# Optimization experiments

Measured on AMD Instinct MI355X. Metric: run time of the kernel, lower is better.

Reference implementation:

```python
import jax, jax.numpy as jnp
import numpy as np

H_RES, W_RES = 32, 32
DIM = 512
NUM_HEADS = 16
HEAD_DIM = DIM // NUM_HEADS
SCALE = HEAD_DIM ** -0.5
B = 16
N = H_RES * W_RES
TABLE_SIZE = (2 * H_RES - 1) * (2 * W_RES - 1)


def _relative_position_index():
    coords_h = np.arange(H_RES)
    coords_w = np.arange(W_RES)
    coords = np.stack(np.meshgrid(coords_h, coords_w, indexing='ij'))  # [2, H, W]
    coords_flat = coords.reshape(2, -1)  # [2, N]
    rel = coords_flat[:, :, None] - coords_flat[:, None, :]  # [2, N, N]
    rel = rel.transpose(1, 2, 0).astype(np.int64)  # [N, N, 2]
    rel[:, :, 0] += H_RES - 1
    rel[:, :, 1] += W_RES - 1
    rel[:, :, 0] *= 2 * W_RES - 1
    return rel.sum(-1)  # [N, N]


def setup_inputs() -> dict:
    key = jax.random.key(0)
    ks = jax.random.split(key, 6)
    x = jax.random.normal(ks[0], (B, N, DIM), dtype=jnp.float32)
    w_qkv = jax.random.normal(ks[1], (DIM, 3 * DIM), dtype=jnp.float32) * (DIM ** -0.5)
    b_qkv = jnp.zeros((3 * DIM,), dtype=jnp.float32)
    w_proj = jax.random.normal(ks[2], (DIM, DIM), dtype=jnp.float32) * (DIM ** -0.5)
    b_proj = jnp.zeros((DIM,), dtype=jnp.float32)
    bias_table = jax.random.normal(ks[3], (TABLE_SIZE, NUM_HEADS), dtype=jnp.float32) * 0.02
    rel_index = jnp.asarray(_relative_position_index(), dtype=jnp.int32)
    return {"x": x, "w_qkv": w_qkv, "b_qkv": b_qkv, "w_proj": w_proj,
            "b_proj": b_proj, "bias_table": bias_table, "rel_index": rel_index}


def reference(x, w_qkv, b_qkv, w_proj, b_proj, bias_table, rel_index):
    Bq, Nq, C = x.shape
    qkv = x @ w_qkv + b_qkv  # [B, N, 3C]
    qkv = qkv.reshape(Bq, Nq, 3, NUM_HEADS, HEAD_DIM)
    q = qkv[:, :, 0].transpose(0, 2, 1, 3) * SCALE  # [B, nH, N, d]
    k = qkv[:, :, 1].transpose(0, 2, 1, 3)
    v = qkv[:, :, 2].transpose(0, 2, 1, 3)
    attn = jnp.einsum('bhnd,bhmd->bhnm', q, k)  # [B, nH, N, N]
    bias = bias_table[rel_index]  # [N, N, nH]
    attn = attn + bias.transpose(2, 0, 1)[None]  # broadcast over batch
    attn = jax.nn.softmax(attn, axis=-1)
    out = jnp.einsum('bhnm,bhmd->bhnd', attn, v)  # [B, nH, N, d]
    out = out.transpose(0, 2, 1, 3).reshape(Bq, Nq, C)
    return out @ w_proj + b_proj
```

## Files before the change

kernel.cpp:

```cpp
#include <hip/hip_runtime.h>
#include <hip/hip_bf16.h>
#include <cstdint>
#include <cstddef>

typedef _Float16 f16;
typedef __attribute__((ext_vector_type(8))) _Float16 f16x8;
typedef __attribute__((ext_vector_type(2))) _Float16 f16x2;
typedef __bf16 bf16;
typedef __attribute__((ext_vector_type(4))) float f32x4;
typedef __attribute__((ext_vector_type(16))) float f32x16;

#define LOG2E 1.4426950408889634f
#define QK_SCALE 0.17677669529663687f

__device__ __forceinline__ f32x4 mfma16f(f16x8 a, f16x8 b, f32x4 c) {
  return __builtin_amdgcn_mfma_f32_16x16x32_f16(a, b, c, 0, 0, 0);
}
__device__ __forceinline__ f32x16 mfma32f(f16x8 a, f16x8 b, f32x16 c) {
  return __builtin_amdgcn_mfma_f32_32x32x16_f16(a, b, c, 0, 0, 0);
}
__device__ __forceinline__ float exp2_hw(float x) {
  float r; asm("v_exp_f32 %0, %1" : "=v"(r) : "v"(x)); return r;
}
__device__ __forceinline__ uint32_t cvtpk_f16(float a, float b) {
  uint32_t r; asm("v_cvt_pkrtz_f16_f32 %0, %1, %2" : "=v"(r) : "v"(a), "v"(b)); return r;
}
__device__ __forceinline__ float lo16f(uint32_t u) { return __uint_as_float(u << 16); }
__device__ __forceinline__ float hi16f(uint32_t u) { return __uint_as_float(u & 0xFFFF0000u); }

__device__ __forceinline__ float dot2acc(uint32_t u, float acc) {
  union { uint32_t x; f16x2 h; } c; c.x = u;
  f16x2 one2 = {(_Float16)1.0f, (_Float16)1.0f};
  return __builtin_amdgcn_fdot2(c.h, one2, acc, false);
}

__device__ __forceinline__ void gl16(const f16* g, f16* l) {
  __builtin_amdgcn_global_load_lds(
      (const __attribute__((address_space(1))) void*)g,
      (__attribute__((address_space(3))) void*)l, 16, 0, 0);
}

__device__ __forceinline__ uint32_t packoff(int m, int k) {
  return (((uint32_t)(m >> 7) * 16u + (uint32_t)(k >> 5)) * 8u + (uint32_t)((m >> 4) & 7)) * 512u
       + (uint32_t)((k >> 3) & 3) * 128u + (uint32_t)(m & 15) * 8u + (uint32_t)(k & 7);
}

__global__ __launch_bounds__(256) void prep_kernel(
    const float* __restrict__ x, const float* __restrict__ wqkv, const float* __restrict__ wproj,
    f16* __restrict__ Xp, f16* __restrict__ Wq, f16* __restrict__ Wp)
{
  const int XT  = 16384 * 512 / 16;
  const int WQT = 1536 * 512 / 16;
  int t = blockIdx.x * 256 + threadIdx.x;
  if (t < XT) {
    uint32_t o = (uint32_t)t * 16u;
    uint32_t blk = o >> 9, rem = o & 511u;
    uint32_t k23 = rem >> 7, r16 = (rem >> 3) & 15u;
    uint32_t i7 = blk & 7u, k5 = (blk >> 3) & 15u, m7 = blk >> 7;
    uint32_t m = m7 * 128u + i7 * 16u + r16;
    uint32_t k = k5 * 32u + k23 * 8u;
    const float* s0 = x + (size_t)m * 512 + k;
    f32x4 a0 = *(const f32x4*)s0;
    f32x4 a1 = *(const f32x4*)(s0 + 4);
    f32x4 b0 = *(const f32x4*)(s0 + 512);
    f32x4 b1 = *(const f32x4*)(s0 + 516);
    f16 ov[16];
    #pragma unroll
    for (int j = 0; j < 4; ++j) {
      ov[j] = (f16)a0[j]; ov[4 + j] = (f16)a1[j];
      ov[8 + j] = (f16)b0[j]; ov[12 + j] = (f16)b1[j];
    }
    *(uint4*)(Xp + o) = *(uint4*)&ov[0];
    *(uint4*)(Xp + o + 8) = *(uint4*)&ov[8];
  } else if (t < XT + WQT) {
    uint32_t o = (uint32_t)(t - XT) * 16u;
    uint32_t blk = o >> 9, rem = o & 511u;
    uint32_t k23 = rem >> 7, r16 = (rem >> 3) & 15u;
    uint32_t i7 = blk & 7u, k5 = (blk >> 3) & 15u, m7 = blk >> 7;
    uint32_t n = m7 * 128u + i7 * 16u + r16;
    uint32_t k = k5 * 32u + k23 * 8u;
    f16 ov[16];
    #pragma unroll
    for (int j = 0; j < 8; ++j) {
      ov[j] = (f16)wqkv[(size_t)(k + j) * 1536 + n];
      ov[8 + j] = (f16)wqkv[(size_t)(k + j) * 1536 + n + 1];
    }
    *(uint4*)(Wq + o) = *(uint4*)&ov[0];
    *(uint4*)(Wq + o + 8) = *(uint4*)&ov[8];
  } else {
    uint32_t o = (uint32_t)(t - XT - WQT) * 16u;
    uint32_t blk = o >> 9, rem = o & 511u;
    uint32_t k23 = rem >> 7, r16 = (rem >> 3) & 15u;
    uint32_t i7 = blk & 7u, k5 = (blk >> 3) & 15u, m7 = blk >> 7;
    uint32_t n = m7 * 128u + i7 * 16u + r16;
    uint32_t k = k5 * 32u + k23 * 8u;
    f16 ov[16];
    #pragma unroll
    for (int j = 0; j < 8; ++j) {
      ov[j] = (f16)wproj[(size_t)(k + j) * 512 + n];
      ov[8 + j] = (f16)wproj[(size_t)(k + j) * 512 + n + 1];
    }
    *(uint4*)(Wp + o) = *(uint4*)&ov[0];
    *(uint4*)(Wp + o + 8) = *(uint4*)&ov[8];
  }
}

__global__ __launch_bounds__(256) void tblT_kernel(
    const float* __restrict__ btab, float* __restrict__ tblT)
{
  int e = blockIdx.x * 256 + threadIdx.x;
  if (e < 3969 * 16) {
    int h = e & 15, i = e >> 4;
    tblT[h * 4000 + i] = btab[e] * LOG2E;
  }
}

__global__ __launch_bounds__(256) void biasC_kernel(
    const float* __restrict__ tblT, bf16* __restrict__ biasC)
{
  int t = blockIdx.x * 256 + threadIdx.x;
  if (t >= 16 * 63 * 64) return;
  int lane = t & 63;
  int sh = t >> 6;
  int s = sh % 63, h = sh / 63;
  int lq = lane & 31, hi5 = lane >> 5;
  const float* row = tblT + h * 4000 + s * 63 + 31 + lq;
  bf16 o[16];
  #pragma unroll
  for (int r = 0; r < 16; ++r) {
    int kx = (r & 3) + 8 * (r >> 2) + 4 * hi5;
    o[r] = (bf16)row[-kx];
  }
  *(uint4*)(biasC + (size_t)t * 16) = *(uint4*)&o[0];
  *(uint4*)(biasC + (size_t)t * 16 + 8) = *(uint4*)&o[8];
}

template<int NB>
__global__ __launch_bounds__(256) void gemm_frag(
    const f16* __restrict__ Ap, const f16* __restrict__ Bp,
    const float* __restrict__ bvec,
    f16* __restrict__ Qp, f16* __restrict__ Kp, f16* __restrict__ Vt,
    float* __restrict__ out)
{
  __shared__ f16 sA[3][4096];
  __shared__ f16 sB[3][4096];
  const int bid = blockIdx.x;
  const int xcd = bid & 7, idx = bid >> 3;
  int mb, nb;
  if (NB == 12) { int q = idx / 12; mb = xcd * 16 + q; nb = idx - q * 12; }
  else          { mb = xcd * 16 + (idx >> 2); nb = idx & 3; }
  const int tid = threadIdx.x, lane = tid & 63, wave = tid >> 6;
  const int l15 = lane & 15, l4 = lane >> 4;
  const int wr = wave >> 1, wc = wave & 1;

  const f16* gA = Ap + (uint32_t)mb * 65536u + (uint32_t)wave * 1024u + (uint32_t)lane * 8u;
  const f16* gB = Bp + (uint32_t)nb * 65536u + (uint32_t)wave * 1024u + (uint32_t)lane * 8u;
  const int wl = wave * 1024;

  gl16(gA,        &sA[0][wl]);
  gl16(gA + 512,  &sA[0][wl + 512]);
  gl16(gB,        &sB[0][wl]);
  gl16(gB + 512,  &sB[0][wl + 512]);
  gl16(gA + 4096, &sA[1][wl]);
  gl16(gA + 4608, &sA[1][wl + 512]);
  gl16(gB + 4096, &sB[1][wl]);
  gl16(gB + 4608, &sB[1][wl + 512]);

  f32x4 acc[4][4];
  #pragma unroll
  for (int i = 0; i < 4; ++i)
    #pragma unroll
    for (int j = 0; j < 4; ++j) acc[i][j] = (f32x4){0.f, 0.f, 0.f, 0.f};

  const uint32_t aoff = (uint32_t)(wr * 4) * 512u + (uint32_t)lane * 8u;
  const uint32_t boff = (uint32_t)(wc * 4) * 512u + (uint32_t)lane * 8u;

  #pragma unroll
  for (int kt = 0; kt < 16; ++kt) {
    asm volatile("s_waitcnt vmcnt(4)" ::: "memory");
    asm volatile("s_barrier" ::: "memory");
    const int s0 = kt % 3;
    f16x8 af[4], bfr[4];
    #pragma unroll
    for (int f = 0; f < 4; ++f) {
      af[f]  = *(const f16x8*)&sA[s0][aoff + f * 512];
      bfr[f] = *(const f16x8*)&sB[s0][boff + f * 512];
    }
    const int s2 = (kt + 2) % 3;
    gl16(gA + (kt + 2) * 4096,       &sA[s2][wl]);
    gl16(gA + (kt + 2) * 4096 + 512, &sA[s2][wl + 512]);
    gl16(gB + (kt + 2) * 4096,       &sB[s2][wl]);
    gl16(gB + (kt + 2) * 4096 + 512, &sB[s2][wl + 512]);
    #pragma unroll
    for (int mf = 0; mf < 4; ++mf)
      #pragma unroll
      for (int nf = 0; nf < 4; ++nf)
        acc[mf][nf] = mfma16f(af[mf], bfr[nf], acc[mf][nf]);
  }
  asm volatile("s_waitcnt vmcnt(0)" ::: "memory");

  #pragma unroll
  for (int mf = 0; mf < 4; ++mf) {
    #pragma unroll
    for (int nf = 0; nf < 4; ++nf) {
      int colb = nb * 128 + wc * 64 + nf * 16 + l15;
      float bb = bvec[colb];
      #pragma unroll
      for (int i = 0; i < 4; ++i) {
        int m = mb * 128 + wr * 64 + mf * 16 + l4 * 4 + i;
        float v = acc[mf][nf][i] + bb;
        if (NB == 4) {
          out[(size_t)m * 512 + colb] = v;
        } else {
          int t = colb >> 9, cc = colb & 511;
          int b = m >> 10, n = m & 1023;
          int hh = cc >> 5, d = cc & 31;
          int bh2 = b * 16 + hh;
          if (t == 0) {
            v *= (QK_SCALE * LOG2E);
            uint32_t off = (((uint32_t)bh2 * 32u + (uint32_t)(n >> 5)) * 2u + (uint32_t)(d >> 4)) * 512u
                         + ((uint32_t)((d >> 3) & 1) * 32u + (uint32_t)(n & 31)) * 8u + (uint32_t)(d & 7);
            Qp[off] = (f16)v;
          } else if (t == 1) {
            Kp[((size_t)(bh2 * 2 + (d >> 4)) * 1024 + n) * 16 + (d & 15)] = (f16)v;
          } else {
            int nl = n & 15;
            int npl = (nl >= 4 && nl < 12) ? (nl ^ 12) : nl;
            int np = (n & ~15) | npl;
            Vt[((size_t)(bh2 * 128 + (np >> 3)) * 32 + d) * 8 + (np & 7)] = (f16)v;
          }
        }
      }
    }
  }
}

__global__ __launch_bounds__(256) void attn_kernel(
    const f16* __restrict__ Qp, const f16* __restrict__ Kp, const f16* __restrict__ Vt,
    const bf16* __restrict__ biasC, f16* __restrict__ Op)
{
  const int bid = blockIdx.x;
  const int xcd = bid & 7, slot = bid >> 3;
  const int h = xcd * 2 + (slot >> 6);
  const int rest = slot & 63;
  const int qg = rest >> 4, b = rest & 15;
  const int bh = b * 16 + h;
  const int tid = threadIdx.x, lane = tid & 63, wave = tid >> 6;
  const int lq = lane & 31, hi5 = lane >> 5;

  const int qb0 = qg * 8 + wave * 2;
  const int m0 = b * 1024 + qb0 * 32;

  const uint32_t qbase = ((uint32_t)bh * 32u + (uint32_t)qb0) * 1024u + (uint32_t)lane * 8u;
  const f16x8 q00 = *(const f16x8*)(Qp + qbase);
  const f16x8 q01 = *(const f16x8*)(Qp + qbase + 512);
  const f16x8 q10 = *(const f16x8*)(Qp + qbase + 1024);
  const f16x8 q11 = *(const f16x8*)(Qp + qbase + 1536);

  uint32_t koff = (uint32_t)bh * 32768u + (uint32_t)lq * 16u + (uint32_t)hi5 * 8u;
  uint32_t voff = (uint32_t)bh * 32768u + (uint32_t)hi5 * 256u + (uint32_t)lq * 8u;
  const bf16* bp = biasC + ((uint32_t)(h * 63 + qb0 + 31) * 64u + (uint32_t)lane) * 16u;

  f16x8 kA0 = *(const f16x8*)(Kp + koff);
  f16x8 kA1 = *(const f16x8*)(Kp + koff + 16384);
  uint4 p0A = *(const uint4*)(bp);
  uint4 p1A = *(const uint4*)(bp + 8);
  uint4 p2A = *(const uint4*)(bp + 1024);
  uint4 p3A = *(const uint4*)(bp + 1032);
  f16x8 vA0 = *(const f16x8*)(Vt + voff);
  f16x8 vA1 = *(const f16x8*)(Vt + voff + 512);
  f16x8 kB0 = *(const f16x8*)(Kp + koff + 512);
  f16x8 kB1 = *(const f16x8*)(Kp + koff + 16384 + 512);
  uint4 p0B = *(const uint4*)(bp - 1024);
  uint4 p1B = *(const uint4*)(bp - 1016);
  uint4 p2B = *(const uint4*)(bp);
  uint4 p3B = *(const uint4*)(bp + 8);
  f16x8 vB0 = *(const f16x8*)(Vt + voff + 1024);
  f16x8 vB1 = *(const f16x8*)(Vt + voff + 1536);

  f32x16 O0, O1;
  #pragma unroll
  for (int i = 0; i < 16; ++i) { O0[i] = 0.f; O1[i] = 0.f; }
  f32x4 racc0 = {0.f, 0.f, 0.f, 0.f}, racc1 = {0.f, 0.f, 0.f, 0.f};

  union Uf { uint32_t u[4]; f16x8 v; };

#define UNPACK16(S, Pa, Pb)                              \
  S[0]  = lo16f(Pa.x); S[1]  = hi16f(Pa.x);              \
  S[2]  = lo16f(Pa.y); S[3]  = hi16f(Pa.y);              \
  S[4]  = lo16f(Pa.z); S[5]  = hi16f(Pa.z);              \
  S[6]  = lo16f(Pa.w); S[7]  = hi16f(Pa.w);              \
  S[8]  = lo16f(Pb.x); S[9]  = hi16f(Pb.x);              \
  S[10] = lo16f(Pb.y); S[11] = hi16f(Pb.y);              \
  S[12] = lo16f(Pb.z); S[13] = hi16f(Pb.z);              \
  S[14] = lo16f(Pb.w); S[15] = hi16f(Pb.w);

  auto tile = [&](f16x8& K0, f16x8& K1, f16x8& V0, f16x8& V1,
                  uint4& P0, uint4& P1, uint4& P2, uint4& P3,
                  uint32_t kpre, uint32_t vpre, int bpre) {
    asm volatile("s_waitcnt vmcnt(8)" ::: "memory");
    f32x16 S0, S1;
    UNPACK16(S0, P0, P1)
    UNPACK16(S1, P2, P3)
    S0 = mfma32f(K0, q00, S0);
    S0 = mfma32f(K1, q01, S0);
    S1 = mfma32f(K0, q10, S1);
    S1 = mfma32f(K1, q11, S1);
    K0 = *(const f16x8*)(Kp + koff + kpre);
    K1 = *(const f16x8*)(Kp + koff + 16384 + kpre);
    P0 = *(const uint4*)(bp + bpre);
    P1 = *(const uint4*)(bp + bpre + 8);
    P2 = *(const uint4*)(bp + bpre + 1024);
    P3 = *(const uint4*)(bp + bpre + 1032);
    __builtin_amdgcn_sched_barrier(0);
    {
      float e0  = exp2_hw(S0[0]),  e1  = exp2_hw(S0[1]),  e2  = exp2_hw(S0[2]),  e3  = exp2_hw(S0[3]);
      float e4  = exp2_hw(S0[4]),  e5  = exp2_hw(S0[5]),  e6  = exp2_hw(S0[6]),  e7  = exp2_hw(S0[7]);
      float e8  = exp2_hw(S0[8]),  e9  = exp2_hw(S0[9]),  e10 = exp2_hw(S0[10]), e11 = exp2_hw(S0[11]);
      float e12 = exp2_hw(S0[12]), e13 = exp2_hw(S0[13]), e14 = exp2_hw(S0[14]), e15 = exp2_hw(S0[15]);
      Uf a1, a2;
      a1.u[0] = cvtpk_f16(e0,  e1);  a1.u[1] = cvtpk_f16(e2,  e3);
      a1.u[2] = cvtpk_f16(e4,  e5);  a1.u[3] = cvtpk_f16(e6,  e7);
      a2.u[0] = cvtpk_f16(e8,  e9);  a2.u[1] = cvtpk_f16(e10, e11);
      a2.u[2] = cvtpk_f16(e12, e13); a2.u[3] = cvtpk_f16(e14, e15);
      racc0[0] = dot2acc(a1.u[0], racc0[0]); racc0[1] = dot2acc(a1.u[1], racc0[1]);
      racc0[2] = dot2acc(a1.u[2], racc0[2]); racc0[3] = dot2acc(a1.u[3], racc0[3]);
      racc0[0] = dot2acc(a2.u[0], racc0[0]); racc0[1] = dot2acc(a2.u[1], racc0[1]);
      racc0[2] = dot2acc(a2.u[2], racc0[2]); racc0[3] = dot2acc(a2.u[3], racc0[3]);
      O0 = mfma32f(a1.v, V0, O0);
      O0 = mfma32f(a2.v, V1, O0);
    }
    {
      float e0  = exp2_hw(S1[0]),  e1  = exp2_hw(S1[1]),  e2  = exp2_hw(S1[2]),  e3  = exp2_hw(S1[3]);
      float e4  = exp2_hw(S1[4]),  e5  = exp2_hw(S1[5]),  e6  = exp2_hw(S1[6]),  e7  = exp2_hw(S1[7]);
      float e8  = exp2_hw(S1[8]),  e9  = exp2_hw(S1[9]),  e10 = exp2_hw(S1[10]), e11 = exp2_hw(S1[11]);
      float e12 = exp2_hw(S1[12]), e13 = exp2_hw(S1[13]), e14 = exp2_hw(S1[14]), e15 = exp2_hw(S1[15]);
      Uf a1, a2;
      a1.u[0] = cvtpk_f16(e0,  e1);  a1.u[1] = cvtpk_f16(e2,  e3);
      a1.u[2] = cvtpk_f16(e4,  e5);  a1.u[3] = cvtpk_f16(e6,  e7);
      a2.u[0] = cvtpk_f16(e8,  e9);  a2.u[1] = cvtpk_f16(e10, e11);
      a2.u[2] = cvtpk_f16(e12, e13); a2.u[3] = cvtpk_f16(e14, e15);
      racc1[0] = dot2acc(a1.u[0], racc1[0]); racc1[1] = dot2acc(a1.u[1], racc1[1]);
      racc1[2] = dot2acc(a1.u[2], racc1[2]); racc1[3] = dot2acc(a1.u[3], racc1[3]);
      racc1[0] = dot2acc(a2.u[0], racc1[0]); racc1[1] = dot2acc(a2.u[1], racc1[1]);
      racc1[2] = dot2acc(a2.u[2], racc1[2]); racc1[3] = dot2acc(a2.u[3], racc1[3]);
      O1 = mfma32f(a1.v, V0, O1);
      O1 = mfma32f(a2.v, V1, O1);
    }
    V0 = *(const f16x8*)(Vt + voff + vpre);
    V1 = *(const f16x8*)(Vt + voff + vpre + 512);
    __builtin_amdgcn_sched_barrier(0);
  };

  #pragma unroll 1
  for (int it = 0; it < 16; ++it) {
    tile(kA0, kA1, vA0, vA1, p0A, p1A, p2A, p3A, 1024u, 2048u, -2048);
    tile(kB0, kB1, vB0, vB1, p0B, p1B, p2B, p3B, 1536u, 3072u, -3072);
    koff += 1024u; voff += 2048u; bp -= 2048;
  }

  float rs0 = (racc0[0] + racc0[1]) + (racc0[2] + racc0[3]);
  rs0 += __shfl_xor(rs0, 32);
  float inv0 = 1.0f / rs0;
  float rs1 = (racc1[0] + racc1[1]) + (racc1[2] + racc1[3]);
  rs1 += __shfl_xor(rs1, 32);
  float inv1 = 1.0f / rs1;

  const int kcol = h * 32 + lq;
  #pragma unroll
  for (int r = 0; r < 16; ++r) {
    int qrow = (r & 3) + 8 * (r >> 2) + 4 * hi5;
    float t0 = __shfl(inv0, qrow);
    float t1 = __shfl(inv1, qrow);
    Op[packoff(m0 + qrow, kcol)] = (f16)(O0[r] * t0);
    Op[packoff(m0 + 32 + qrow, kcol)] = (f16)(O1[r] * t1);
  }
}

extern "C" void kernel_launch(void* const* d_in, const int* in_sizes, int n_in,
                              void* d_out, int out_size, void* d_ws, size_t ws_size,
                              hipStream_t stream) {
  const float* x     = (const float*)d_in[0];
  const float* wqkv  = (const float*)d_in[1];
  const float* bqkv  = (const float*)d_in[2];
  const float* wproj = (const float*)d_in[3];
  const float* bproj = (const float*)d_in[4];
  const float* btab  = (const float*)d_in[5];
  float* out = (float*)d_out;

  char* ws = (char*)d_ws;
  size_t off = 0;
  auto walloc = [&](size_t bytes) {
    void* p = ws + off;
    off += (bytes + 255) & ~(size_t)255;
    return p;
  };
  const size_t PAD = 262144;
  f16* Xp   = (f16*)walloc((size_t)16384 * 512 * 2 + PAD);
  f16* Wq   = (f16*)walloc((size_t)1536 * 512 * 2 + PAD);
  f16* Wp   = (f16*)walloc((size_t)512 * 512 * 2 + PAD);
  float* tblT = (float*)walloc((size_t)16 * 4000 * 4);
  f16* Qp   = (f16*)walloc((size_t)16384 * 512 * 2 + PAD);
  f16* Kp   = (f16*)walloc((size_t)16384 * 512 * 2 + PAD);
  f16* Vt   = (f16*)walloc((size_t)16384 * 512 * 2 + PAD);
  bf16* biasC = (bf16*)walloc((size_t)16 * 63 * 64 * 16 * 2 + PAD);
  f16* Op   = (f16*)walloc((size_t)16384 * 512 * 2 + PAD);

  const int prep_blocks = (16384 * 512 / 16 + 1536 * 512 / 16 + 512 * 512 / 16) / 256;
  prep_kernel<<<prep_blocks, 256, 0, stream>>>(x, wqkv, wproj, Xp, Wq, Wp);

  tblT_kernel<<<(3969 * 16 + 255) / 256, 256, 0, stream>>>(btab, tblT);

  biasC_kernel<<<(16 * 63 * 64 + 255) / 256, 256, 0, stream>>>(tblT, biasC);

  gemm_frag<12><<<1536, 256, 0, stream>>>(
      Xp, Wq, bqkv, Qp, Kp, Vt, nullptr);

  attn_kernel<<<1024, 256, 0, stream>>>(Qp, Kp, Vt, biasC, Op);

  gemm_frag<4><<<512, 256, 0, stream>>>(
      Op, Wp, bproj, nullptr, nullptr, nullptr, out);
}
```

Measured before the change: 159.9 us.

## Fuse bias table transpose into biasC, reorder GEMM prefetch, drop hi-half mask

Removes the separate tblT kernel and its workspace buffer, so biasC reads the bias table directly with a strided gather and applies the log2e scale inline. In the GEMM main loop the global-to-LDS prefetch is now issued before the LDS fragment reads, with a sched_barrier so the compiler keeps that order. The attention bias unpack no longer masks the low 16 bits when widening the high bf16 half, which saves one ALU op per element but leaves a small low-mantissa perturbation in the bias value. The aim is one fewer launch and less instruction overhead, at the cost of an uncoalesced gather in biasC.

```diff
diff --git a/kernel.cpp b/kernel.cpp
--- a/kernel.cpp
+++ b/kernel.cpp
@@ -26,7 +26,7 @@
   uint32_t r; asm("v_cvt_pkrtz_f16_f32 %0, %1, %2" : "=v"(r) : "v"(a), "v"(b)); return r;
 }
 __device__ __forceinline__ float lo16f(uint32_t u) { return __uint_as_float(u << 16); }
-__device__ __forceinline__ float hi16f(uint32_t u) { return __uint_as_float(u & 0xFFFF0000u); }
+__device__ __forceinline__ float hi16raw(uint32_t u) { return __uint_as_float(u); }
 
 __device__ __forceinline__ float dot2acc(uint32_t u, float acc) {
   union { uint32_t x; f16x2 h; } c; c.x = u;
@@ -105,18 +105,8 @@
   }
 }
 
-__global__ __launch_bounds__(256) void tblT_kernel(
-    const float* __restrict__ btab, float* __restrict__ tblT)
-{
-  int e = blockIdx.x * 256 + threadIdx.x;
-  if (e < 3969 * 16) {
-    int h = e & 15, i = e >> 4;
-    tblT[h * 4000 + i] = btab[e] * LOG2E;
-  }
-}
-
 __global__ __launch_bounds__(256) void biasC_kernel(
-    const float* __restrict__ tblT, bf16* __restrict__ biasC)
+    const float* __restrict__ btab, bf16* __restrict__ biasC)
 {
   int t = blockIdx.x * 256 + threadIdx.x;
   if (t >= 16 * 63 * 64) return;
@@ -124,12 +114,12 @@
   int sh = t >> 6;
   int s = sh % 63, h = sh / 63;
   int lq = lane & 31, hi5 = lane >> 5;
-  const float* row = tblT + h * 4000 + s * 63 + 31 + lq;
+  int base = s * 63 + 31 + lq;
   bf16 o[16];
   #pragma unroll
   for (int r = 0; r < 16; ++r) {
     int kx = (r & 3) + 8 * (r >> 2) + 4 * hi5;
-    o[r] = (bf16)row[-kx];
+    o[r] = (bf16)(btab[(base - kx) * 16 + h] * LOG2E);
   }
   *(uint4*)(biasC + (size_t)t * 16) = *(uint4*)&o[0];
   *(uint4*)(biasC + (size_t)t * 16 + 8) = *(uint4*)&o[8];
@@ -179,18 +169,19 @@
   for (int kt = 0; kt < 16; ++kt) {
     asm volatile("s_waitcnt vmcnt(4)" ::: "memory");
     asm volatile("s_barrier" ::: "memory");
-    const int s0 = kt % 3;
-    f16x8 af[4], bfr[4];
-    #pragma unroll
-    for (int f = 0; f < 4; ++f) {
-      af[f]  = *(const f16x8*)&sA[s0][aoff + f * 512];
-      bfr[f] = *(const f16x8*)&sB[s0][boff + f * 512];
-    }
     const int s2 = (kt + 2) % 3;
     gl16(gA + (kt + 2) * 4096,       &sA[s2][wl]);
     gl16(gA + (kt + 2) * 4096 + 512, &sA[s2][wl + 512]);
     gl16(gB + (kt + 2) * 4096,       &sB[s2][wl]);
     gl16(gB + (kt + 2) * 4096 + 512, &sB[s2][wl + 512]);
+    __builtin_amdgcn_sched_barrier(0);
+    const int s0 = kt % 3;
+    f16x8 af[4], bfr[4];
+    #pragma unroll
+    for (int f = 0; f < 4; ++f) {
+      af[f]  = *(const f16x8*)&sA[s0][aoff + f * 512];
+      bfr[f] = *(const f16x8*)&sB[s0][boff + f * 512];
+    }
     #pragma unroll
     for (int mf = 0; mf < 4; ++mf)
       #pragma unroll
@@ -285,15 +276,15 @@
 
   union Uf { uint32_t u[4]; f16x8 v; };
 
-#define UNPACK16(S, Pa, Pb)                              \
-  S[0]  = lo16f(Pa.x); S[1]  = hi16f(Pa.x);              \
-  S[2]  = lo16f(Pa.y); S[3]  = hi16f(Pa.y);              \
-  S[4]  = lo16f(Pa.z); S[5]  = hi16f(Pa.z);              \
-  S[6]  = lo16f(Pa.w); S[7]  = hi16f(Pa.w);              \
-  S[8]  = lo16f(Pb.x); S[9]  = hi16f(Pb.x);              \
-  S[10] = lo16f(Pb.y); S[11] = hi16f(Pb.y);              \
-  S[12] = lo16f(Pb.z); S[13] = hi16f(Pb.z);              \
-  S[14] = lo16f(Pb.w); S[15] = hi16f(Pb.w);
+#define UNPACK16(S, Pa, Pb)                               \
+  S[0]  = lo16f(Pa.x); S[1]  = hi16raw(Pa.x);             \
+  S[2]  = lo16f(Pa.y); S[3]  = hi16raw(Pa.y);             \
+  S[4]  = lo16f(Pa.z); S[5]  = hi16raw(Pa.z);             \
+  S[6]  = lo16f(Pa.w); S[7]  = hi16raw(Pa.w);             \
+  S[8]  = lo16f(Pb.x); S[9]  = hi16raw(Pb.x);             \
+  S[10] = lo16f(Pb.y); S[11] = hi16raw(Pb.y);             \
+  S[12] = lo16f(Pb.z); S[13] = hi16raw(Pb.z);             \
+  S[14] = lo16f(Pb.w); S[15] = hi16raw(Pb.w);
 
   auto tile = [&](f16x8& K0, f16x8& K1, f16x8& V0, f16x8& V1,
                   uint4& P0, uint4& P1, uint4& P2, uint4& P3,
@@ -399,7 +390,6 @@
   f16* Xp   = (f16*)walloc((size_t)16384 * 512 * 2 + PAD);
   f16* Wq   = (f16*)walloc((size_t)1536 * 512 * 2 + PAD);
   f16* Wp   = (f16*)walloc((size_t)512 * 512 * 2 + PAD);
-  float* tblT = (float*)walloc((size_t)16 * 4000 * 4);
   f16* Qp   = (f16*)walloc((size_t)16384 * 512 * 2 + PAD);
   f16* Kp   = (f16*)walloc((size_t)16384 * 512 * 2 + PAD);
   f16* Vt   = (f16*)walloc((size_t)16384 * 512 * 2 + PAD);
@@ -409,9 +399,7 @@
   const int prep_blocks = (16384 * 512 / 16 + 1536 * 512 / 16 + 512 * 512 / 16) / 256;
   prep_kernel<<<prep_blocks, 256, 0, stream>>>(x, wqkv, wproj, Xp, Wq, Wp);
 
-  tblT_kernel<<<(3969 * 16 + 255) / 256, 256, 0, stream>>>(btab, tblT);
-
-  biasC_kernel<<<(16 * 63 * 64 + 255) / 256, 256, 0, stream>>>(tblT, biasC);
+  biasC_kernel<<<(16 * 63 * 64 + 255) / 256, 256, 0, stream>>>(btab, biasC);
 
   gemm_frag<12><<<1536, 256, 0, stream>>>(
       Xp, Wq, bqkv, Qp, Kp, Vt, nullptr);
```

Measured after the change: 150.5 us. -5.8%, faster.
